# Kernel optimization log

Measured on AMD Instinct MI355X. Metric: run time of the kernel, lower is better.

Reference implementation:

```python
import jax, jax.numpy as jnp
import numpy as np

WS = 8
NH = 6

def _ln(x, g, b, eps=1e-5):
    m = x.mean(-1, keepdims=True)
    v = jnp.var(x, axis=-1, keepdims=True)
    return (x - m) / jnp.sqrt(v + eps) * g + b

def _dwconv(x_nchw, k):
    # depthwise 3x3, stride 1, padding 1 (SAME); k: (C,1,3,3)
    return jax.lax.conv_general_dilated(
        x_nchw, k, (1, 1), 'SAME',
        dimension_numbers=('NCHW', 'OIHW', 'NCHW'),
        feature_group_count=x_nchw.shape[1])

def setup_inputs() -> dict:
    key = jax.random.key(0)
    ks = jax.random.split(key, 12)
    B, H, W, C = 2, 256, 256, 180
    hd_ffn = 360
    s = 0.02
    return {
        'x': jax.random.normal(ks[0], (B, H * W, C), jnp.float32),
        'w_qkv': jax.random.normal(ks[1], (3 * C, C), jnp.float32) * s,
        'b_rel': jax.random.normal(ks[2], (NH, WS * WS, WS * WS), jnp.float32) * s,
        'w_proj': jax.random.normal(ks[3], (C, C), jnp.float32) * s,
        'b_proj': jnp.zeros((C,), jnp.float32),
        'conv_dw': jax.random.normal(ks[4], (C, 1, 3, 3), jnp.float32) * 0.1,
        'cg_w1': jax.random.normal(ks[5], (C // 8, C), jnp.float32) * s,
        'cg_w2': jax.random.normal(ks[6], (C, C // 8), jnp.float32) * s,
        'ffn_w1': jax.random.normal(ks[7], (hd_ffn, C), jnp.float32) * s,
        'ffn_dw': jax.random.normal(ks[8], (hd_ffn, 1, 3, 3), jnp.float32) * 0.1,
        'ffn_w2': jax.random.normal(ks[9], (C, hd_ffn), jnp.float32) * s,
        'n1_g': jnp.ones((C,), jnp.float32),
        'n1_b': jnp.zeros((C,), jnp.float32),
        'n2_g': jnp.ones((C,), jnp.float32),
        'n2_b': jnp.zeros((C,), jnp.float32),
        'H': H,
        'W': W,
    }

def reference(x, w_qkv, b_rel, w_proj, b_proj, conv_dw, cg_w1, cg_w2,
              ffn_w1, ffn_dw, ffn_w2, n1_g, n1_b, n2_g, n2_b, H, W):
    B, L, C = x.shape
    hd = C // NH
    scale = hd ** -0.5
    n1 = _ln(x, n1_g, n1_b)
    # --- spatial window attention branch ---
    xw = n1.reshape(B, H // WS, WS, W // WS, WS, C)
    xw = xw.transpose(0, 1, 3, 2, 4, 5).reshape(-1, WS * WS, C)  # (nw, 64, C)
    qkv = (xw @ w_qkv.T).reshape(-1, WS * WS, 3, NH, hd).transpose(2, 0, 3, 1, 4)
    q, k, v = qkv[0], qkv[1], qkv[2]  # (nw, nh, 64, hd)
    attn = jax.nn.softmax((q * scale) @ jnp.swapaxes(k, -2, -1) + b_rel, axis=-1)
    out = (attn @ v).transpose(0, 2, 1, 3).reshape(-1, WS * WS, C)
    out = out @ w_proj.T + b_proj
    attn_feat = out.reshape(B, H // WS, W // WS, WS, WS, C)
    attn_feat = attn_feat.transpose(0, 1, 3, 2, 4, 5).reshape(B, L, C)
    # --- conv branch: depthwise 3x3 + GELU ---
    nchw = n1.transpose(0, 2, 1).reshape(B, C, H, W)
    conv_feat = jax.nn.gelu(_dwconv(nchw, conv_dw), approximate=False)
    conv_feat = conv_feat.reshape(B, C, L).transpose(0, 2, 1)
    # --- AIM: channel gate on conv_feat modulates attn_feat ---
    pooled = conv_feat.mean(axis=1)  # (B, C) == AdaptiveAvgPool2d(1)
    cm = jax.nn.sigmoid(jax.nn.gelu(pooled @ cg_w1.T, approximate=False) @ cg_w2.T)
    x = x + (attn_feat * cm[:, None, :] + conv_feat)
    # --- FFN with depthwise spatial mixing ---
    n2 = _ln(x, n2_g, n2_b)
    h = jax.nn.gelu(n2 @ ffn_w1.T, approximate=False)  # (B, L, hd_ffn)
    hdim = h.shape[-1]
    h_s = _dwconv(h.transpose(0, 2, 1).reshape(B, hdim, H, W), ffn_dw)
    h_s = h_s.reshape(B, hdim, L).transpose(0, 2, 1)
    return x + h_s @ ffn_w2.T
```

## Files before the change

kernel.cpp:

```cpp
#include <hip/hip_runtime.h>
#include <hip/hip_bf16.h>
#include <math.h>

#define BATCH 2
#define IMG 256
#define LTOK 65536
#define CH 180
#define BL (BATCH * LTOK)
#define HDF 360

using frag_ab = __attribute__((ext_vector_type(8))) short;
using frag_cd = __attribute__((ext_vector_type(4))) float;

__device__ __forceinline__ float b2f(unsigned short u) {
    union { unsigned int i; float f; } v; v.i = ((unsigned int)u) << 16; return v.f;
}
__device__ __forceinline__ float blo(unsigned int u) {
    union { unsigned int i; float f; } v; v.i = u << 16; return v.f;
}
__device__ __forceinline__ float bhi(unsigned int u) {
    union { unsigned int i; float f; } v; v.i = u & 0xffff0000u; return v.f;
}
__device__ __forceinline__ unsigned short f2b(float f) {
    union { float f; unsigned int i; } v; v.f = f;
    unsigned int x = v.i;
    unsigned int r = (x + 0x7fffu + ((x >> 16) & 1u)) >> 16;
    return (unsigned short)r;
}
__device__ __forceinline__ float gelu_f(float x) {
    return 0.5f * x * (1.0f + erff(x * 0.70710678118654752f));
}

template <int PERM>
__device__ __forceinline__ int perm_row(int row) {
    if (PERM == 1) {
        int b = row >> 16, l = row & 65535;
        int y = l >> 8, x = l & 255;
        return (b << 16) + ((((y >> 3) << 5) + (x >> 3)) << 6) + ((y & 7) << 3) + (x & 7);
    } else if (PERM == 2) {
        int b = row >> 16, wv = row & 65535;
        int wid = wv >> 6, t = wv & 63;
        int wy = wid >> 5, wx = wid & 31;
        return (b << 16) + ((((wy << 3) + (t >> 3))) << 8) + (wx << 3) + (t & 7);
    }
    return row;
}

__global__ __launch_bounds__(256) void convw_kernel(
    const float* __restrict__ a, const float* __restrict__ b,
    const float* __restrict__ c, const float* __restrict__ d,
    const float* __restrict__ cdw, const float* __restrict__ fdw,
    const float* __restrict__ brel,
    unsigned short* __restrict__ wbf, float* __restrict__ wT1, float* __restrict__ wT2,
    unsigned short* __restrict__ br3)
{
    int g = blockIdx.x * 256 + threadIdx.x;
    if (g < 259200) {
        float v;
        if      (g < 97200)  v = a[g];
        else if (g < 129600) v = b[g - 97200];
        else if (g < 194400) v = c[g - 129600];
        else                 v = d[g - 194400];
        wbf[g] = f2b(v);
    } else if (g < 265680) {
        int i = g - 259200;
        int tap = i / 180, ch = i % 180;
        wT1[i] = cdw[ch * 9 + tap];
    } else if (g < 278640) {
        int i = g - 265680;
        int tap = i / 360, ch = i % 360;
        wT2[i] = fdw[ch * 9 + tap];
    } else if (g < 303216) {
        int i = g - 278640;
        int h = i >> 12;
        int rem = i & 4095;
        int lane = rem >> 6;
        int j = rem & 63;
        int mt = j >> 4, nt = (j >> 2) & 3, r = j & 3;
        int row = mt * 16 + (lane >> 4) * 4 + r;
        int col = nt * 16 + (lane & 15);
        br3[i] = f2b(brel[h * 4096 + row * 64 + col]);
    }
}

__device__ __forceinline__ void ld4(const float* p, float v[4]) {
    float4 t = *(const float4*)p; v[0]=t.x; v[1]=t.y; v[2]=t.z; v[3]=t.w;
}
__device__ __forceinline__ void ld4(const unsigned short* p, float v[4]) {
    ushort4 t = *(const ushort4*)p; v[0]=b2f(t.x); v[1]=b2f(t.y); v[2]=b2f(t.z); v[3]=b2f(t.w);
}

template <typename TIN>
__global__ __launch_bounds__(256) void ln_kernel(
    const TIN* __restrict__ x, const float* __restrict__ g,
    const float* __restrict__ bta, unsigned short* __restrict__ out)
{
    int wave = threadIdx.x >> 6, lane = threadIdx.x & 63;
    int tok = blockIdx.x * 4 + wave;
    const bool act = lane < 45;
    float v[4] = {0.f, 0.f, 0.f, 0.f};
    const TIN* row = x + (size_t)tok * CH;
    if (act) ld4(row + lane * 4, v);
    float s  = v[0] + v[1] + v[2] + v[3];
    float sq = v[0]*v[0] + v[1]*v[1] + v[2]*v[2] + v[3]*v[3];
    #pragma unroll
    for (int off = 32; off > 0; off >>= 1) {
        s  += __shfl_xor(s, off);
        sq += __shfl_xor(sq, off);
    }
    float mean = s * (1.f / CH);
    float var  = sq * (1.f / CH) - mean * mean;
    float rstd = rsqrtf(var + 1e-5f);
    if (act) {
        float4 gg = *(const float4*)&g[lane * 4];
        float4 bb = *(const float4*)&bta[lane * 4];
        unsigned int o0 = (unsigned int)f2b((v[0]-mean)*rstd*gg.x + bb.x)
                        | ((unsigned int)f2b((v[1]-mean)*rstd*gg.y + bb.y) << 16);
        unsigned int o1 = (unsigned int)f2b((v[2]-mean)*rstd*gg.z + bb.z)
                        | ((unsigned int)f2b((v[3]-mean)*rstd*gg.w + bb.w) << 16);
        *(uint2*)(out + (size_t)tok * CH + lane * 4) = make_uint2(o0, o1);
    }
}

__device__ __forceinline__ void stv(float* p, float v) { *p = v; }
__device__ __forceinline__ void stv(unsigned short* p, float v) { *p = f2b(v); }

template <int ACT, bool HAS_BIAS, bool HAS_RES, int PERM, typename TOUT>
__global__ __launch_bounds__(256) void gemm_kernel(
    const unsigned short* __restrict__ X, int ldx,
    const unsigned short* __restrict__ Wt,
    const float* __restrict__ bias,
    const unsigned short* __restrict__ res, int ldr,
    TOUT* __restrict__ Y, int ldy,
    int N, int K)
{
    __shared__ unsigned short Xs[64][40];
    __shared__ unsigned short Ws[64][40];
    const int tid = threadIdx.x;
    const int wave = tid >> 6;
    const int lane = tid & 63;
    const int l16 = lane & 15;
    const int q = lane >> 4;
    const int m0 = blockIdx.x * 64;
    const int n0 = blockIdx.y * 64;
    const int lr = tid >> 2;
    const int lk = (tid & 3) << 3;

    frag_cd acc[4];
    #pragma unroll
    for (int i = 0; i < 4; ++i) acc[i] = (frag_cd){0.f, 0.f, 0.f, 0.f};

    for (int k0 = 0; k0 < K; k0 += 32) {
        const bool kfull = (k0 + 32 <= K);
        {
            const unsigned short* p = X + (size_t)(m0 + lr) * ldx + (k0 + lk);
            if (kfull) {
                *(uint2*)&Xs[lr][lk]     = *(const uint2*)p;
                *(uint2*)&Xs[lr][lk + 4] = *(const uint2*)(p + 4);
            } else {
                #pragma unroll
                for (int j = 0; j < 8; ++j)
                    Xs[lr][lk + j] = (k0 + lk + j < K) ? p[j] : (unsigned short)0;
            }
        }
        {
            const int n = n0 + lr;
            const unsigned short* p = Wt + (size_t)n * K + (k0 + lk);
            if (n < N && kfull) {
                *(uint2*)&Ws[lr][lk]     = *(const uint2*)p;
                *(uint2*)&Ws[lr][lk + 4] = *(const uint2*)(p + 4);
            } else {
                #pragma unroll
                for (int j = 0; j < 8; ++j)
                    Ws[lr][lk + j] = (n < N && (k0 + lk + j) < K) ? p[j] : (unsigned short)0;
            }
        }
        __syncthreads();
        frag_ab bfr = *(const frag_ab*)&Ws[wave * 16 + l16][q * 8];
        #pragma unroll
        for (int mb = 0; mb < 4; ++mb) {
            frag_ab afr = *(const frag_ab*)&Xs[mb * 16 + l16][q * 8];
            acc[mb] = __builtin_amdgcn_mfma_f32_16x16x32_bf16(afr, bfr, acc[mb], 0, 0, 0);
        }
        __syncthreads();
    }
    const int col = n0 + wave * 16 + l16;
    if (col < N) {
        float bv = 0.f;
        if (HAS_BIAS) bv = bias[col];
        #pragma unroll
        for (int mb = 0; mb < 4; ++mb) {
            #pragma unroll
            for (int r = 0; r < 4; ++r) {
                int row = m0 + mb * 16 + q * 4 + r;
                int orow = perm_row<PERM>(row);
                float v = acc[mb][r] + bv;
                if (ACT == 1) v = gelu_f(v);
                if (HAS_RES) v += b2f(res[(size_t)orow * ldr + col]);
                stv(&Y[(size_t)orow * ldy + col], v);
            }
        }
    }
}

__global__ __launch_bounds__(64) void attn_kernel(
    const unsigned short* __restrict__ qkvw,
    const unsigned short* __restrict__ br3,
    unsigned short* __restrict__ attn_out)
{
    __shared__ unsigned short Pl[64][72];
    __shared__ unsigned short VT[32][72];
    const int blk = blockIdx.x;
    const int h = blk % 6;
    const int w = blk / 6;
    const int lane = threadIdx.x;
    const int l16 = lane & 15;
    const int g4 = lane >> 4;
    const float scale = 0.18257418583505536f;

    const unsigned short* base = qkvw + (size_t)w * (64 * 540) + h * 30;

    frag_ab qf[4], kf[4];
    #pragma unroll
    for (int t = 0; t < 4; ++t) {
        const unsigned short* pq = base + (size_t)(t * 16 + l16) * 540 + g4 * 8;
        union { frag_ab f; uint2 u[2]; } tq, tk;
        tq.u[0] = *(const uint2*)pq;        tq.u[1] = *(const uint2*)(pq + 4);
        tk.u[0] = *(const uint2*)(pq + 180); tk.u[1] = *(const uint2*)(pq + 184);
        if (g4 == 3) { tk.f[6] = 0; tk.f[7] = 0; }
        qf[t] = tq.f; kf[t] = tk.f;
    }

    unsigned int brw[32];
    {
        const unsigned short* bp = br3 + ((size_t)h << 12) + lane * 64;
        #pragma unroll
        for (int c2 = 0; c2 < 8; ++c2)
            *(uint4*)&brw[c2 * 4] = *(const uint4*)(bp + c2 * 8);
    }

    frag_cd s[4][4];
    #pragma unroll
    for (int mt = 0; mt < 4; ++mt)
        #pragma unroll
        for (int nt = 0; nt < 4; ++nt)
            s[mt][nt] = (frag_cd){0.f, 0.f, 0.f, 0.f};
    #pragma unroll
    for (int mt = 0; mt < 4; ++mt)
        #pragma unroll
        for (int nt = 0; nt < 4; ++nt)
            s[mt][nt] = __builtin_amdgcn_mfma_f32_16x16x32_bf16(qf[mt], kf[nt], s[mt][nt], 0, 0, 0);

    {
        const unsigned short* pv = base + (size_t)lane * 540 + 360;
        #pragma unroll
        for (int d2 = 0; d2 < 15; ++d2) {
            unsigned int u = *(const unsigned int*)(pv + 2 * d2);
            VT[2 * d2][lane]     = (unsigned short)(u & 0xffffu);
            VT[2 * d2 + 1][lane] = (unsigned short)(u >> 16);
        }
        VT[30][lane] = 0; VT[31][lane] = 0;
    }

    float inv[4][4];
    #pragma unroll
    for (int mt = 0; mt < 4; ++mt) {
        #pragma unroll
        for (int r = 0; r < 4; ++r) {
            float a0 = s[mt][0][r] * scale + (((0 * 4 + r) & 1) ? bhi(brw[(mt * 16 + 0 + r) >> 1]) : blo(brw[(mt * 16 + 0 + r) >> 1]));
            float a1 = s[mt][1][r] * scale + (((1 * 4 + r) & 1) ? bhi(brw[(mt * 16 + 4 + r) >> 1]) : blo(brw[(mt * 16 + 4 + r) >> 1]));
            float a2 = s[mt][2][r] * scale + (((2 * 4 + r) & 1) ? bhi(brw[(mt * 16 + 8 + r) >> 1]) : blo(brw[(mt * 16 + 8 + r) >> 1]));
            float a3 = s[mt][3][r] * scale + (((3 * 4 + r) & 1) ? bhi(brw[(mt * 16 + 12 + r) >> 1]) : blo(brw[(mt * 16 + 12 + r) >> 1]));
            float m = fmaxf(fmaxf(a0, a1), fmaxf(a2, a3));
            m = fmaxf(m, __shfl_xor(m, 1));
            m = fmaxf(m, __shfl_xor(m, 2));
            m = fmaxf(m, __shfl_xor(m, 4));
            m = fmaxf(m, __shfl_xor(m, 8));
            float e0 = __expf(a0 - m), e1 = __expf(a1 - m);
            float e2 = __expf(a2 - m), e3 = __expf(a3 - m);
            float sum = e0 + e1 + e2 + e3;
            sum += __shfl_xor(sum, 1);
            sum += __shfl_xor(sum, 2);
            sum += __shfl_xor(sum, 4);
            sum += __shfl_xor(sum, 8);
            inv[mt][r] = 1.f / sum;
            int row = mt * 16 + g4 * 4 + r;
            Pl[row][l16]      = f2b(e0);
            Pl[row][16 + l16] = f2b(e1);
            Pl[row][32 + l16] = f2b(e2);
            Pl[row][48 + l16] = f2b(e3);
        }
    }
    __syncthreads();

    frag_ab pf[4][2];
    #pragma unroll
    for (int mt = 0; mt < 4; ++mt)
        #pragma unroll
        for (int kt = 0; kt < 2; ++kt)
            pf[mt][kt] = *(const frag_ab*)&Pl[mt * 16 + l16][kt * 32 + g4 * 8];
    frag_ab vf[2][2];
    #pragma unroll
    for (int nt = 0; nt < 2; ++nt)
        #pragma unroll
        for (int kt = 0; kt < 2; ++kt)
            vf[nt][kt] = *(const frag_ab*)&VT[nt * 16 + l16][kt * 32 + g4 * 8];

    frag_cd o[4][2];
    #pragma unroll
    for (int mt = 0; mt < 4; ++mt)
        #pragma unroll
        for (int nt = 0; nt < 2; ++nt)
            o[mt][nt] = (frag_cd){0.f, 0.f, 0.f, 0.f};
    #pragma unroll
    for (int mt = 0; mt < 4; ++mt)
        #pragma unroll
        for (int nt = 0; nt < 2; ++nt)
            #pragma unroll
            for (int kt = 0; kt < 2; ++kt)
                o[mt][nt] = __builtin_amdgcn_mfma_f32_16x16x32_bf16(pf[mt][kt], vf[nt][kt], o[mt][nt], 0, 0, 0);

    unsigned short* ob = attn_out + (size_t)w * (64 * CH) + h * 30;
    #pragma unroll
    for (int mt = 0; mt < 4; ++mt) {
        #pragma unroll
        for (int r = 0; r < 4; ++r) {
            int row = mt * 16 + g4 * 4 + r;
            float iv = inv[mt][r];
            unsigned short* op = ob + (size_t)row * CH;
            op[l16] = f2b(o[mt][0][r] * iv);
            if (l16 < 14) op[16 + l16] = f2b(o[mt][1][r] * iv);
        }
    }
}

template <int C, bool DO_GELU>
__global__ __launch_bounds__(256) void dwconv_kernel(
    const unsigned short* __restrict__ in, const float* __restrict__ wT,
    unsigned short* __restrict__ out)
{
    constexpr int NG = (C + 7) / 8;
    constexpr int TY = 8;
    int gid = blockIdx.x * 256 + threadIdx.x;
    int cg = gid % NG;
    int t  = gid / NG;
    int x  = t % IMG;
    int t2 = t / IMG;
    int yb = t2 & 31;
    int bi = t2 >> 5;
    if (bi >= BATCH) return;
    const int c0 = cg * 8;
    const int y0 = yb * TY;

    float w9[9][8];
    #pragma unroll
    for (int tp = 0; tp < 9; ++tp) {
        float4 wa = *(const float4*)&wT[tp * C + c0];
        float4 wb = *(const float4*)&wT[tp * C + c0 + 4];
        w9[tp][0]=wa.x; w9[tp][1]=wa.y; w9[tp][2]=wa.z; w9[tp][3]=wa.w;
        w9[tp][4]=wb.x; w9[tp][5]=wb.y; w9[tp][6]=wb.z; w9[tp][7]=wb.w;
    }

    unsigned int rr[3][3][4];

    auto load_row = [&](int y, unsigned int dst[3][4]) {
        if ((unsigned)y >= (unsigned)IMG) {
            #pragma unroll
            for (int cc = 0; cc < 3; ++cc)
                #pragma unroll
                for (int k = 0; k < 4; ++k) dst[cc][k] = 0u;
            return;
        }
        size_t base = ((size_t)((bi << 16) + (y << 8) + x)) * C + c0;
        #pragma unroll
        for (int cc = 0; cc < 3; ++cc) {
            int xx = x + cc - 1;
            if ((unsigned)xx >= (unsigned)IMG) {
                dst[cc][0] = dst[cc][1] = dst[cc][2] = dst[cc][3] = 0u;
                continue;
            }
            const unsigned short* p = in + base + (ptrdiff_t)(cc - 1) * C;
            uint2 u0 = *(const uint2*)p;
            uint2 u1 = *(const uint2*)(p + 4);
            dst[cc][0] = u0.x; dst[cc][1] = u0.y; dst[cc][2] = u1.x; dst[cc][3] = u1.y;
        }
    };

    load_row(y0 - 1, rr[0]);
    load_row(y0,     rr[1]);

    #pragma unroll
    for (int dy = 0; dy < TY; ++dy) {
        load_row(y0 + dy + 1, rr[(dy + 2) % 3]);
        float acc[8];
        #pragma unroll
        for (int j = 0; j < 8; ++j) acc[j] = 0.f;
        #pragma unroll
        for (int ky = 0; ky < 3; ++ky) {
            unsigned int (*row)[4] = rr[(dy + ky) % 3];
            #pragma unroll
            for (int kx = 0; kx < 3; ++kx) {
                const float* wp = w9[ky * 3 + kx];
                const unsigned int* u = row[kx];
                acc[0] += blo(u[0]) * wp[0];
                acc[1] += bhi(u[0]) * wp[1];
                acc[2] += blo(u[1]) * wp[2];
                acc[3] += bhi(u[1]) * wp[3];
                acc[4] += blo(u[2]) * wp[4];
                acc[5] += bhi(u[2]) * wp[5];
                acc[6] += blo(u[3]) * wp[6];
                acc[7] += bhi(u[3]) * wp[7];
            }
        }
        if (DO_GELU) {
            #pragma unroll
            for (int j = 0; j < 8; ++j) acc[j] = gelu_f(acc[j]);
        }
        size_t ob = ((size_t)((bi << 16) + ((y0 + dy) << 8) + x)) * C + c0;
        unsigned int o0 = (unsigned int)f2b(acc[0]) | ((unsigned int)f2b(acc[1]) << 16);
        unsigned int o1 = (unsigned int)f2b(acc[2]) | ((unsigned int)f2b(acc[3]) << 16);
        *(uint2*)(out + ob) = make_uint2(o0, o1);
        if (c0 + 8 <= C) {
            unsigned int o2 = (unsigned int)f2b(acc[4]) | ((unsigned int)f2b(acc[5]) << 16);
            unsigned int o3 = (unsigned int)f2b(acc[6]) | ((unsigned int)f2b(acc[7]) << 16);
            *(uint2*)(out + ob + 4) = make_uint2(o2, o3);
        }
    }
}

__global__ __launch_bounds__(64) void pool_kernel(
    const unsigned short* __restrict__ cf, float* __restrict__ pooled)
{
    int t = threadIdx.x;
    if (t >= 45) return;
    int b = blockIdx.x >> 7;
    int chunk = blockIdx.x & 127;
    const unsigned short* base = cf + (size_t)(b * LTOK + chunk * 512) * CH + t * 4;
    float s0 = 0.f, s1 = 0.f, s2 = 0.f, s3 = 0.f;
    for (int i = 0; i < 512; ++i) {
        ushort4 v = *(const ushort4*)(base + (size_t)i * CH);
        s0 += b2f(v.x); s1 += b2f(v.y); s2 += b2f(v.z); s3 += b2f(v.w);
    }
    atomicAdd(&pooled[b * CH + t * 4 + 0], s0);
    atomicAdd(&pooled[b * CH + t * 4 + 1], s1);
    atomicAdd(&pooled[b * CH + t * 4 + 2], s2);
    atomicAdd(&pooled[b * CH + t * 4 + 3], s3);
}

__global__ __launch_bounds__(256) void cm_kernel(
    const float* __restrict__ pooled, const float* __restrict__ w1,
    const float* __restrict__ w2, float* __restrict__ cm)
{
    __shared__ float p[BATCH][CH];
    __shared__ float g1[BATCH][22];
    int t = threadIdx.x;
    for (int idx = t; idx < BATCH * CH; idx += 256)
        p[idx / CH][idx % CH] = pooled[idx] * (1.f / (float)LTOK);
    __syncthreads();
    if (t < BATCH * 22) {
        int b = t / 22, u = t % 22;
        float s = 0.f;
        for (int c = 0; c < CH; ++c) s += p[b][c] * w1[u * CH + c];
        g1[b][u] = gelu_f(s);
    }
    __syncthreads();
    for (int idx = t; idx < BATCH * CH; idx += 256) {
        int b = idx / CH, c = idx % CH;
        float s = 0.f;
        for (int u = 0; u < 22; ++u) s += g1[b][u] * w2[c * 22 + u];
        cm[idx] = 1.f / (1.f + __expf(-s));
    }
}

__global__ __launch_bounds__(256) void resid_kernel(
    const float* __restrict__ x, const unsigned short* __restrict__ attn_feat,
    const unsigned short* __restrict__ conv_feat, const float* __restrict__ cm,
    unsigned short* __restrict__ x_mid)
{
    int gid = blockIdx.x * 256 + threadIdx.x;
    int c4 = gid % 45;
    int b = gid / (LTOK * 45);
    float4 xv = ((const float4*)x)[gid];
    ushort4 a = ((const ushort4*)attn_feat)[gid];
    ushort4 c = ((const ushort4*)conv_feat)[gid];
    float4 m = *(const float4*)&cm[b * CH + c4 * 4];
    unsigned int o0 = (unsigned int)f2b(xv.x + b2f(a.x) * m.x + b2f(c.x))
                    | ((unsigned int)f2b(xv.y + b2f(a.y) * m.y + b2f(c.y)) << 16);
    unsigned int o1 = (unsigned int)f2b(xv.z + b2f(a.z) * m.z + b2f(c.z))
                    | ((unsigned int)f2b(xv.w + b2f(a.w) * m.w + b2f(c.w)) << 16);
    ((uint2*)x_mid)[gid] = make_uint2(o0, o1);
}

extern "C" void kernel_launch(void* const* d_in, const int* in_sizes, int n_in,
                              void* d_out, int out_size, void* d_ws, size_t ws_size,
                              hipStream_t stream)
{
    const float* x       = (const float*)d_in[0];
    const float* w_qkv   = (const float*)d_in[1];
    const float* b_rel   = (const float*)d_in[2];
    const float* w_proj  = (const float*)d_in[3];
    const float* b_proj  = (const float*)d_in[4];
    const float* conv_dw = (const float*)d_in[5];
    const float* cg_w1   = (const float*)d_in[6];
    const float* cg_w2   = (const float*)d_in[7];
    const float* ffn_w1  = (const float*)d_in[8];
    const float* ffn_dw  = (const float*)d_in[9];
    const float* ffn_w2  = (const float*)d_in[10];
    const float* n1_g    = (const float*)d_in[11];
    const float* n1_b    = (const float*)d_in[12];
    const float* n2_g    = (const float*)d_in[13];
    const float* n2_b    = (const float*)d_in[14];

    char* ws = (char*)d_ws;
    unsigned short* n1        = (unsigned short*)(ws);
    unsigned short* qkvw      = (unsigned short*)(ws + 47185920);
    unsigned short* conv_feat = (unsigned short*)(ws + 188743680);
    unsigned short* attn_out  = (unsigned short*)(ws);
    unsigned short* attn_feat = (unsigned short*)(ws + 47185920);
    unsigned short* x_mid     = (unsigned short*)(ws + 94371840);
    unsigned short* n2        = (unsigned short*)(ws + 141557760);
    unsigned short* h         = (unsigned short*)(ws);
    unsigned short* h_s       = (unsigned short*)(ws + 141557760);
    float*          pooled    = (float*)(ws + 235929600);
    float*          cmv       = (float*)(ws + 235931040);
    unsigned short* wbf       = (unsigned short*)(ws + 235932480);
    float*          wT1       = (float*)(ws + 236450880);
    float*          wT2       = (float*)(ws + 236476800);
    unsigned short* br3       = (unsigned short*)(ws + 236528640);
    unsigned short* wqkv_b  = wbf;
    unsigned short* wproj_b = wbf + 97200;
    unsigned short* wffn1_b = wbf + 129600;
    unsigned short* wffn2_b = wbf + 194400;
    float* out = (float*)d_out;

    hipMemsetAsync(pooled, 0, 2880, stream);

    convw_kernel<<<1185, 256, 0, stream>>>(w_qkv, w_proj, ffn_w1, ffn_w2,
                                           conv_dw, ffn_dw, b_rel, wbf, wT1, wT2, br3);
    ln_kernel<float><<<BL / 4, 256, 0, stream>>>(x, n1_g, n1_b, n1);
    gemm_kernel<0, false, false, 1, unsigned short><<<dim3(BL / 64, 9), 256, 0, stream>>>(
        n1, CH, wqkv_b, nullptr, nullptr, 0, qkvw, 540, 540, CH);
    dwconv_kernel<CH, true><<<1472, 256, 0, stream>>>(n1, wT1, conv_feat);
    pool_kernel<<<BATCH * 128, 64, 0, stream>>>(conv_feat, pooled);
    cm_kernel<<<1, 256, 0, stream>>>(pooled, cg_w1, cg_w2, cmv);
    attn_kernel<<<2048 * 6, 64, 0, stream>>>(qkvw, br3, attn_out);
    gemm_kernel<0, true, false, 2, unsigned short><<<dim3(BL / 64, 3), 256, 0, stream>>>(
        attn_out, CH, wproj_b, b_proj, nullptr, 0, attn_feat, CH, CH, CH);
    resid_kernel<<<(BL * CH / 4) / 256, 256, 0, stream>>>(x, attn_feat, conv_feat, cmv, x_mid);
    ln_kernel<unsigned short><<<BL / 4, 256, 0, stream>>>(x_mid, n2_g, n2_b, n2);
    gemm_kernel<1, false, false, 0, unsigned short><<<dim3(BL / 64, 6), 256, 0, stream>>>(
        n2, CH, wffn1_b, nullptr, nullptr, 0, h, HDF, HDF, CH);
    dwconv_kernel<HDF, false><<<2880, 256, 0, stream>>>(h, wT2, h_s);
    gemm_kernel<0, false, true, 0, float><<<dim3(BL / 64, 3), 256, 0, stream>>>(
        h_s, HDF, wffn2_b, nullptr, x_mid, CH, out, CH, CH, HDF);
}
```

Measured before the change: 952.5 us.

## Enlarge GEMM tile to 256x64 with 4x4 MFMA fragments per wave

The GEMM block tile grows from 64x64 to 256x64 rows, and each wave now computes a 64x64 sub-tile with a 4x4 grid of MFMA accumulators instead of a single 16-column strip. The launch grid is transposed so blockIdx.x walks the N tiles, which lets blocks sharing the same X rows run next to each other for L2 reuse. LDS stores are widened to 16-byte writes. The aim is more MFMA work per LDS load and per barrier, at the cost of more accumulator registers (64 floats) and more LDS per block, which may lower occupancy.

```diff
diff --git a/kernel.cpp b/kernel.cpp
--- a/kernel.cpp
+++ b/kernel.cpp
@@ -134,41 +134,48 @@
     TOUT* __restrict__ Y, int ldy,
     int N, int K)
 {
-    __shared__ unsigned short Xs[64][40];
+    __shared__ unsigned short Xs[256][40];
     __shared__ unsigned short Ws[64][40];
     const int tid = threadIdx.x;
     const int wave = tid >> 6;
     const int lane = tid & 63;
     const int l16 = lane & 15;
     const int q = lane >> 4;
-    const int m0 = blockIdx.x * 64;
-    const int n0 = blockIdx.y * 64;
+    const int n0 = blockIdx.x * 64;
+    const int m0 = blockIdx.y * 256;
     const int lr = tid >> 2;
     const int lk = (tid & 3) << 3;
 
-    frag_cd acc[4];
-    #pragma unroll
-    for (int i = 0; i < 4; ++i) acc[i] = (frag_cd){0.f, 0.f, 0.f, 0.f};
+    frag_cd acc[4][4];
+    #pragma unroll
+    for (int mb = 0; mb < 4; ++mb)
+        #pragma unroll
+        for (int nb = 0; nb < 4; ++nb)
+            acc[mb][nb] = (frag_cd){0.f, 0.f, 0.f, 0.f};
 
     for (int k0 = 0; k0 < K; k0 += 32) {
         const bool kfull = (k0 + 32 <= K);
-        {
-            const unsigned short* p = X + (size_t)(m0 + lr) * ldx + (k0 + lk);
+        #pragma unroll
+        for (int rr = 0; rr < 4; ++rr) {
+            const int row = rr * 64 + lr;
+            const unsigned short* p = X + (size_t)(m0 + row) * ldx + (k0 + lk);
             if (kfull) {
-                *(uint2*)&Xs[lr][lk]     = *(const uint2*)p;
-                *(uint2*)&Xs[lr][lk + 4] = *(const uint2*)(p + 4);
+                uint2 u0 = *(const uint2*)p;
+                uint2 u1 = *(const uint2*)(p + 4);
+                *(uint4*)&Xs[row][lk] = make_uint4(u0.x, u0.y, u1.x, u1.y);
             } else {
                 #pragma unroll
                 for (int j = 0; j < 8; ++j)
-                    Xs[lr][lk + j] = (k0 + lk + j < K) ? p[j] : (unsigned short)0;
+                    Xs[row][lk + j] = (k0 + lk + j < K) ? p[j] : (unsigned short)0;
             }
         }
         {
             const int n = n0 + lr;
             const unsigned short* p = Wt + (size_t)n * K + (k0 + lk);
             if (n < N && kfull) {
-                *(uint2*)&Ws[lr][lk]     = *(const uint2*)p;
-                *(uint2*)&Ws[lr][lk + 4] = *(const uint2*)(p + 4);
+                uint2 u0 = *(const uint2*)p;
+                uint2 u1 = *(const uint2*)(p + 4);
+                *(uint4*)&Ws[lr][lk] = make_uint4(u0.x, u0.y, u1.x, u1.y);
             } else {
                 #pragma unroll
                 for (int j = 0; j < 8; ++j)
@@ -176,28 +183,36 @@
             }
         }
         __syncthreads();
-        frag_ab bfr = *(const frag_ab*)&Ws[wave * 16 + l16][q * 8];
+        frag_ab bfr[4];
+        #pragma unroll
+        for (int nb = 0; nb < 4; ++nb)
+            bfr[nb] = *(const frag_ab*)&Ws[nb * 16 + l16][q * 8];
         #pragma unroll
         for (int mb = 0; mb < 4; ++mb) {
-            frag_ab afr = *(const frag_ab*)&Xs[mb * 16 + l16][q * 8];
-            acc[mb] = __builtin_amdgcn_mfma_f32_16x16x32_bf16(afr, bfr, acc[mb], 0, 0, 0);
+            frag_ab afr = *(const frag_ab*)&Xs[wave * 64 + mb * 16 + l16][q * 8];
+            #pragma unroll
+            for (int nb = 0; nb < 4; ++nb)
+                acc[mb][nb] = __builtin_amdgcn_mfma_f32_16x16x32_bf16(afr, bfr[nb], acc[mb][nb], 0, 0, 0);
         }
         __syncthreads();
     }
-    const int col = n0 + wave * 16 + l16;
-    if (col < N) {
-        float bv = 0.f;
-        if (HAS_BIAS) bv = bias[col];
-        #pragma unroll
-        for (int mb = 0; mb < 4; ++mb) {
+    #pragma unroll
+    for (int nb = 0; nb < 4; ++nb) {
+        const int col = n0 + nb * 16 + l16;
+        if (col < N) {
+            float bv = 0.f;
+            if (HAS_BIAS) bv = bias[col];
             #pragma unroll
-            for (int r = 0; r < 4; ++r) {
-                int row = m0 + mb * 16 + q * 4 + r;
-                int orow = perm_row<PERM>(row);
-                float v = acc[mb][r] + bv;
-                if (ACT == 1) v = gelu_f(v);
-                if (HAS_RES) v += b2f(res[(size_t)orow * ldr + col]);
-                stv(&Y[(size_t)orow * ldy + col], v);
+            for (int mb = 0; mb < 4; ++mb) {
+                #pragma unroll
+                for (int r = 0; r < 4; ++r) {
+                    int row = m0 + wave * 64 + mb * 16 + q * 4 + r;
+                    int orow = perm_row<PERM>(row);
+                    float v = acc[mb][nb][r] + bv;
+                    if (ACT == 1) v = gelu_f(v);
+                    if (HAS_RES) v += b2f(res[(size_t)orow * ldr + col]);
+                    stv(&Y[(size_t)orow * ldy + col], v);
+                }
             }
         }
     }
@@ -538,19 +553,19 @@
     convw_kernel<<<1185, 256, 0, stream>>>(w_qkv, w_proj, ffn_w1, ffn_w2,
                                            conv_dw, ffn_dw, b_rel, wbf, wT1, wT2, br3);
     ln_kernel<float><<<BL / 4, 256, 0, stream>>>(x, n1_g, n1_b, n1);
-    gemm_kernel<0, false, false, 1, unsigned short><<<dim3(BL / 64, 9), 256, 0, stream>>>(
+    gemm_kernel<0, false, false, 1, unsigned short><<<dim3(9, BL / 256), 256, 0, stream>>>(
         n1, CH, wqkv_b, nullptr, nullptr, 0, qkvw, 540, 540, CH);
     dwconv_kernel<CH, true><<<1472, 256, 0, stream>>>(n1, wT1, conv_feat);
     pool_kernel<<<BATCH * 128, 64, 0, stream>>>(conv_feat, pooled);
     cm_kernel<<<1, 256, 0, stream>>>(pooled, cg_w1, cg_w2, cmv);
     attn_kernel<<<2048 * 6, 64, 0, stream>>>(qkvw, br3, attn_out);
-    gemm_kernel<0, true, false, 2, unsigned short><<<dim3(BL / 64, 3), 256, 0, stream>>>(
+    gemm_kernel<0, true, false, 2, unsigned short><<<dim3(3, BL / 256), 256, 0, stream>>>(
         attn_out, CH, wproj_b, b_proj, nullptr, 0, attn_feat, CH, CH, CH);
     resid_kernel<<<(BL * CH / 4) / 256, 256, 0, stream>>>(x, attn_feat, conv_feat, cmv, x_mid);
     ln_kernel<unsigned short><<<BL / 4, 256, 0, stream>>>(x_mid, n2_g, n2_b, n2);
-    gemm_kernel<1, false, false, 0, unsigned short><<<dim3(BL / 64, 6), 256, 0, stream>>>(
+    gemm_kernel<1, false, false, 0, unsigned short><<<dim3(6, BL / 256), 256, 0, stream>>>(
         n2, CH, wffn1_b, nullptr, nullptr, 0, h, HDF, HDF, CH);
     dwconv_kernel<HDF, false><<<2880, 256, 0, stream>>>(h, wT2, h_s);
-    gemm_kernel<0, false, true, 0, float><<<dim3(BL / 64, 3), 256, 0, stream>>>(
+    gemm_kernel<0, false, true, 0, float><<<dim3(3, BL / 256), 256, 0, stream>>>(
         h_s, HDF, wffn2_b, nullptr, x_mid, CH, out, CH, CH, HDF);
 }
```

Result: slower. 1.052 ms (+10.4%).
